# Optimization experiments

Hardware: AMD Instinct MI355X
Metric: run time of the kernel (lower is better)

The kernel has to match this reference:

```python
import jax, jax.numpy as jnp
import numpy as np

N_NODES = 100000
N_EDGES = 1600000
D = 128
N_LAYERS = 3
N_GRAPHS = 64
BN_EPS = 1e-5


def setup_inputs() -> dict:
    key = jax.random.key(0)
    ks = jax.random.split(key, 8)
    x = jax.random.normal(ks[0], (N_NODES, D), dtype=jnp.float32)
    edge_index = jax.random.randint(ks[1], (2, N_EDGES), 0, N_NODES, dtype=jnp.int64)
    batch = jnp.sort(jax.random.randint(ks[2], (N_NODES,), 0, N_GRAPHS, dtype=jnp.int64))
    scale = 1.0 / np.sqrt(D)
    W1 = jax.random.normal(ks[3], (N_LAYERS, D, D), dtype=jnp.float32) * scale
    W2 = jax.random.normal(ks[4], (N_LAYERS, D, D), dtype=jnp.float32) * scale
    g1 = jnp.ones((N_LAYERS, D), dtype=jnp.float32)
    b1 = jnp.zeros((N_LAYERS, D), dtype=jnp.float32)
    g2 = jnp.ones((N_LAYERS, D), dtype=jnp.float32)
    b2 = jnp.zeros((N_LAYERS, D), dtype=jnp.float32)
    eps = jnp.zeros((N_LAYERS,), dtype=jnp.float32)
    return {"x": x, "edge_index": edge_index, "batch": batch,
            "W1": W1, "g1": g1, "b1": b1, "W2": W2, "g2": g2, "b2": b2, "eps": eps}


def _batchnorm(z, gamma, beta):
    # BatchNorm1d in training mode: biased variance over the node dimension.
    mu = jnp.mean(z, axis=0, keepdims=True)
    var = jnp.mean(jnp.square(z - mu), axis=0, keepdims=True)
    return (z - mu) * jax.lax.rsqrt(var + BN_EPS) * gamma + beta


def reference(x, edge_index, batch, W1, g1, b1, W2, g2, b2, eps):
    src, dst = edge_index[0], edge_index[1]
    h = x
    for l in range(N_LAYERS):
        # GIN aggregation: sum of neighbor features via edge-index scatter-add
        agg = jax.ops.segment_sum(h[src], dst, num_segments=N_NODES)
        z = (1.0 + eps[l]) * h + agg
        # MLP: Linear(no bias) -> BN -> ReLU -> Linear(no bias) -> BN
        z = _batchnorm(z @ W1[l], g1[l], b1[l])
        z = jax.nn.relu(z)
        z = _batchnorm(z @ W2[l], g2[l], b2[l])
        h = jax.nn.relu(z)  # gnn_non_linear
    node_emb = h
    # mean readout per graph
    counts = jax.ops.segment_sum(jnp.ones((N_NODES,), dtype=h.dtype), batch, num_segments=N_GRAPHS)
    graph_sum = jax.ops.segment_sum(h, batch, num_segments=N_GRAPHS)
    graph_emb = graph_sum / jnp.maximum(counts, 1.0)[:, None]
    # emb_normalize -> F.normalize(p=2, dim=-1)
    graph_emb = graph_emb / jnp.maximum(jnp.linalg.norm(graph_emb, axis=-1, keepdims=True), 1e-12)
    return node_emb, graph_emb
```

## Files before the change

### kernel.cpp

```cpp
#include <hip/hip_runtime.h>

#define N_NODES 100000
#define N_EDGES 1600000
#define D 128
#define N_GRAPHS 64
#define BN_EPS 1e-5f
#define NSLICE 16

#define BNODES 256
#define NBUCK ((N_NODES + BNODES - 1) / BNODES)
#define EPB 8192
#define NABLK ((N_EDGES + EPB - 1) / EPB)

typedef short short8 __attribute__((ext_vector_type(8)));
typedef float f32x4 __attribute__((ext_vector_type(4)));

__device__ inline unsigned short f2bf(float f) {
  unsigned int u = __float_as_uint(f);
  u += 0x7fffu + ((u >> 16) & 1);
  return (unsigned short)(u >> 16);
}
__device__ inline float bf2f(unsigned short h) {
  return __uint_as_float(((unsigned int)h) << 16);
}
__device__ inline void unpack8(uint4 u, float* f) {
  f[0] = __uint_as_float(u.x << 16); f[1] = __uint_as_float(u.x & 0xffff0000u);
  f[2] = __uint_as_float(u.y << 16); f[3] = __uint_as_float(u.y & 0xffff0000u);
  f[4] = __uint_as_float(u.z << 16); f[5] = __uint_as_float(u.z & 0xffff0000u);
  f[6] = __uint_as_float(u.w << 16); f[7] = __uint_as_float(u.w & 0xffff0000u);
}
__device__ inline uint4 pack8(const float* f) {
  uint4 u;
  u.x = f2bf(f[0]) | ((unsigned)f2bf(f[1]) << 16);
  u.y = f2bf(f[2]) | ((unsigned)f2bf(f[3]) << 16);
  u.z = f2bf(f[4]) | ((unsigned)f2bf(f[5]) << 16);
  u.w = f2bf(f[6]) | ((unsigned)f2bf(f[7]) << 16);
  return u;
}

__global__ __launch_bounds__(256) void k_cast(const float* __restrict__ in,
                                              unsigned short* __restrict__ o) {
  long i = ((long)blockIdx.x * blockDim.x + threadIdx.x) * 8;
  if (i >= (long)N_NODES * D) return;
  float4 a = *(const float4*)(in + i);
  float4 b = *(const float4*)(in + i + 4);
  float f[8] = {a.x, a.y, a.z, a.w, b.x, b.y, b.z, b.w};
  *(uint4*)(o + i) = pack8(f);
}

__global__ __launch_bounds__(128) void k_wprep(const float* __restrict__ W1,
                                               const float* __restrict__ W2,
                                               unsigned short* __restrict__ Wt) {
  int m = blockIdx.x;
  int n = blockIdx.y;
  int k = threadIdx.x;
  int l = m >> 1, s = m & 1;
  const float* W = (s == 0 ? W1 : W2) + (size_t)l * D * D;
  Wt[((size_t)m * D + n) * D + k] = f2bf(W[(size_t)k * D + n]);
}

__global__ __launch_bounds__(256) void k_histb(const int* __restrict__ dst,
                                               int* __restrict__ ecount) {
  __shared__ int lh[NBUCK];
  const int t = threadIdx.x;
  const int e0 = blockIdx.x * EPB;
  const int e1 = min(e0 + EPB, N_EDGES);
  for (int i = t; i < NBUCK; i += 256) lh[i] = 0;
  __syncthreads();
  for (int e = e0 + t; e < e1; e += 256) atomicAdd(&lh[dst[e] >> 8], 1);
  __syncthreads();
  for (int i = t; i < NBUCK; i += 256)
    if (lh[i]) atomicAdd(&ecount[i], lh[i]);
}

__global__ __launch_bounds__(512) void k_scanb(const int* __restrict__ ecount,
                                               int* __restrict__ ebase,
                                               int* __restrict__ gcur) {
  __shared__ int ls[512];
  int t = threadIdx.x;
  int v = (t < NBUCK) ? ecount[t] : 0;
  ls[t] = v;
  __syncthreads();
  for (int o = 1; o < 512; o <<= 1) {
    int u = (t >= o) ? ls[t - o] : 0;
    __syncthreads();
    ls[t] += u;
    __syncthreads();
  }
  int ex = ls[t] - v;
  if (t < NBUCK) { ebase[t] = ex; gcur[t] = ex; }
  if (t == 0) ebase[NBUCK] = N_EDGES;
}

__global__ __launch_bounds__(256) void k_scatA(const int* __restrict__ ei,
                                               int* __restrict__ gcur,
                                               int2* __restrict__ pairs) {
  __shared__ int lh[NBUCK];
  __shared__ int lbase[NBUCK];
  const int t = threadIdx.x;
  const int e0 = blockIdx.x * EPB;
  const int e1 = min(e0 + EPB, N_EDGES);
  for (int i = t; i < NBUCK; i += 256) lh[i] = 0;
  __syncthreads();
  for (int e = e0 + t; e < e1; e += 256) atomicAdd(&lh[ei[N_EDGES + e] >> 8], 1);
  __syncthreads();
  for (int i = t; i < NBUCK; i += 256)
    lbase[i] = (lh[i] > 0) ? atomicAdd(&gcur[i], lh[i]) : 0;
  __syncthreads();
  for (int e = e0 + t; e < e1; e += 256) {
    int s = ei[e];
    int d = ei[N_EDGES + e];
    int p = atomicAdd(&lbase[d >> 8], 1);
    pairs[p] = make_int2(s, d);
  }
}

__global__ __launch_bounds__(256) void k_scatB(const int2* __restrict__ pairs,
                                               const int* __restrict__ ebase,
                                               int* __restrict__ off,
                                               int* __restrict__ esrc) {
  __shared__ int lcnt[BNODES];
  __shared__ int ls[256];
  const int t = threadIdx.x;
  const int b = blockIdx.x;
  const int nb0 = b * BNODES;
  const int nn = min(BNODES, N_NODES - nb0);
  const int s0 = ebase[b], s1 = ebase[b + 1];
  if (t < nn) lcnt[t] = 0;
  __syncthreads();
  for (int e = s0 + t; e < s1; e += 256) atomicAdd(&lcnt[pairs[e].y - nb0], 1);
  __syncthreads();
  int c0 = (t < nn) ? lcnt[t] : 0;
  ls[t] = c0;
  __syncthreads();
  for (int o = 1; o < 256; o <<= 1) {
    int u = (t >= o) ? ls[t - o] : 0;
    __syncthreads();
    ls[t] += u;
    __syncthreads();
  }
  int pre = ls[t] - c0;
  if (t < nn) {
    off[nb0 + t] = s0 + pre;
    lcnt[t] = s0 + pre;
  }
  __syncthreads();
  for (int e = s0 + t; e < s1; e += 256) {
    int2 p = pairs[e];
    int pos = atomicAdd(&lcnt[p.y - nb0], 1);
    esrc[pos] = p.x;
  }
  if (b == 0 && t == 0) off[N_NODES] = N_EDGES;
}

__global__ __launch_bounds__(256) void k_aggz(const unsigned short* __restrict__ h,
                                              const int* __restrict__ off,
                                              const int* __restrict__ esrc,
                                              const float* __restrict__ epsp,
                                              unsigned short* __restrict__ z) {
  const int lane = threadIdx.x & 63;
  const int n = blockIdx.x * 4 + (threadIdx.x >> 6);
  const int es = lane >> 4;
  const int fl = lane & 15;
  const int c = fl << 3;
  const float e = 1.0f + epsp[0];
  const int o0 = off[n], o1 = off[n + 1];

  float acc[8];
#pragma unroll
  for (int q = 0; q < 8; q++) acc[q] = 0.f;

  int j = o0;
  for (; j + 4 <= o1; j += 4) {
    int s = esrc[j + es];
    uint4 u = *(const uint4*)(h + (size_t)s * D + c);
    float f[8];
    unpack8(u, f);
#pragma unroll
    for (int q = 0; q < 8; q++) acc[q] += f[q];
  }
  if (es < o1 - j) {
    int s = esrc[j + es];
    uint4 u = *(const uint4*)(h + (size_t)s * D + c);
    float f[8];
    unpack8(u, f);
#pragma unroll
    for (int q = 0; q < 8; q++) acc[q] += f[q];
  }
#pragma unroll
  for (int q = 0; q < 8; q++) {
    acc[q] += __shfl_xor(acc[q], 16, 64);
    acc[q] += __shfl_xor(acc[q], 32, 64);
  }
  {
    uint4 u = *(const uint4*)(h + (size_t)n * D + c);
    float f[8];
    unpack8(u, f);
#pragma unroll
    for (int q = 0; q < 8; q++) acc[q] = fmaf(e, f[q], acc[q]);
  }
  if (es == 0) *(uint4*)(z + (size_t)n * D + c) = pack8(acc);
}

__global__ __launch_bounds__(256) void k_ew(const unsigned short* __restrict__ y,
                                            const float* __restrict__ sc,
                                            const float* __restrict__ tb,
                                            unsigned short* __restrict__ o) {
  long i = ((long)blockIdx.x * 256 + threadIdx.x) * 8;
  if (i >= (long)N_NODES * D) return;
  int cb = (int)(i & 127);
  uint4 u = *(const uint4*)(y + i);
  float f[8];
  unpack8(u, f);
#pragma unroll
  for (int q = 0; q < 8; q++) f[q] = fmaxf(fmaf(f[q], sc[cb + q], tb[cb + q]), 0.f);
  *(uint4*)(o + i) = pack8(f);
}

template <int MODE>
__global__ __launch_bounds__(256) void k_gemm(const unsigned short* __restrict__ A,
                                              const unsigned short* __restrict__ Wt,
                                              unsigned short* __restrict__ out,
                                              const float* __restrict__ sc,
                                              const float* __restrict__ tb,
                                              float* __restrict__ ssum,
                                              float* __restrict__ ssq) {
  __shared__ unsigned short Zs[64 * 136];
  __shared__ float psum[16 * 128];
  __shared__ float psq[16 * 128];
  const int t = threadIdx.x;
  const int row0 = blockIdx.x * 64;

#pragma unroll
  for (int i = 0; i < 4; i++) {
    int q = t + i * 256;
    int r = q >> 4, cb = (q & 15) << 3;
    int grow = row0 + r;
    uint4 u = make_uint4(0u, 0u, 0u, 0u);
    if (grow < N_NODES) {
      u = *(const uint4*)(A + (size_t)grow * D + cb);
      if (MODE == 1) {
        float f[8];
        unpack8(u, f);
#pragma unroll
        for (int jj = 0; jj < 8; jj++)
          f[jj] = fmaxf(fmaf(f[jj], sc[cb + jj], tb[cb + jj]), 0.f);
        u = pack8(f);
      }
    }
    *(uint4*)&Zs[r * 136 + cb] = u;
  }
  __syncthreads();

  const int lane = t & 63;
  const int wave = t >> 6;
  const int quad = lane >> 4;
  const int lr = lane & 15;
  const int m0 = wave * 16;

  f32x4 acc[8];
#pragma unroll
  for (int i = 0; i < 8; i++) acc[i] = (f32x4){0.f, 0.f, 0.f, 0.f};

#pragma unroll
  for (int kc = 0; kc < 128; kc += 32) {
    short8 af = *(const short8*)&Zs[(m0 + lr) * 136 + kc + quad * 8];
#pragma unroll
    for (int nt = 0; nt < 8; nt++) {
      short8 bf = *(const short8*)(Wt + (size_t)(nt * 16 + lr) * D + kc + quad * 8);
      acc[nt] = __builtin_amdgcn_mfma_f32_16x16x32_bf16(af, bf, acc[nt], 0, 0, 0);
    }
  }

#pragma unroll
  for (int nt = 0; nt < 8; nt++) {
    int col = nt * 16 + lr;
    float s = acc[nt][0] + acc[nt][1] + acc[nt][2] + acc[nt][3];
    float qq = acc[nt][0] * acc[nt][0] + acc[nt][1] * acc[nt][1] +
               acc[nt][2] * acc[nt][2] + acc[nt][3] * acc[nt][3];
    int gi = (wave * 4 + quad) * 128 + col;
    psum[gi] = s;
    psq[gi] = qq;
  }

#pragma unroll
  for (int rr = 0; rr < 4; rr++) {
    int grow = row0 + m0 + quad * 4 + rr;
    if (grow < N_NODES) {
#pragma unroll
      for (int nt = 0; nt < 8; nt++)
        out[(size_t)grow * D + nt * 16 + lr] = f2bf(acc[nt][rr]);
    }
  }

  __syncthreads();
  if (t < 128) {
    float S = 0.f, Q = 0.f;
#pragma unroll
    for (int i = 0; i < 16; i++) {
      S += psum[i * 128 + t];
      Q += psq[i * 128 + t];
    }
    int slice = blockIdx.x & (NSLICE - 1);
    atomicAdd(&ssum[slice * 128 + t], S);
    atomicAdd(&ssq[slice * 128 + t], Q);
  }
}

__global__ void k_bnfin(const float* __restrict__ ssum, const float* __restrict__ ssq,
                        const float* __restrict__ gamma, const float* __restrict__ beta,
                        float* __restrict__ sc, float* __restrict__ tb) {
  int f = threadIdx.x;
  float S = 0.f, Q = 0.f;
  for (int i = 0; i < NSLICE; i++) { S += ssum[i * 128 + f]; Q += ssq[i * 128 + f]; }
  float m = S * (1.0f / (float)N_NODES);
  float v = Q * (1.0f / (float)N_NODES) - m * m;
  float r = rsqrtf(v + BN_EPS);
  float s = r * gamma[f];
  sc[f] = s;
  tb[f] = beta[f] - m * s;
}

#define RCH 64
__global__ __launch_bounds__(128) void k_readout(const unsigned short* __restrict__ y,
                                                 const int* __restrict__ batch,
                                                 const float* __restrict__ sc,
                                                 const float* __restrict__ tb,
                                                 float* __restrict__ node_out,
                                                 float* __restrict__ gsum,
                                                 int* __restrict__ gcnt) {
  int start = blockIdx.x * RCH;
  int end = min(start + RCH, N_NODES);
  if (start >= end) return;
  int f = threadIdx.x;
  float s = sc[f], tt = tb[f];
  float acc = 0.f;
  int cnt = 0;
  int curg = batch[start];
  for (int n = start; n < end; n++) {
    int gg = batch[n];
    float v = fmaxf(fmaf(bf2f(y[(size_t)n * D + f]), s, tt), 0.f);
    node_out[(size_t)n * D + f] = v;
    if (gg != curg) {
      atomicAdd(&gsum[curg * D + f], acc);
      if (f == 0) atomicAdd(&gcnt[curg], cnt);
      acc = 0.f; cnt = 0; curg = gg;
    }
    acc += v;
    cnt++;
  }
  atomicAdd(&gsum[curg * D + f], acc);
  if (f == 0) atomicAdd(&gcnt[curg], cnt);
}

__global__ __launch_bounds__(128) void k_gnorm(const float* __restrict__ gsum,
                                               const int* __restrict__ gcnt,
                                               float* __restrict__ out) {
  __shared__ float red[128];
  int g = blockIdx.x, f = threadIdx.x;
  float c = (float)gcnt[g];
  float v = gsum[g * D + f] / fmaxf(c, 1.0f);
  red[f] = v * v;
  __syncthreads();
  for (int o = 64; o > 0; o >>= 1) {
    if (f < o) red[f] += red[f + o];
    __syncthreads();
  }
  float nrm = sqrtf(red[0]);
  out[(size_t)g * D + f] = v / fmaxf(nrm, 1e-12f);
}

extern "C" void kernel_launch(void* const* d_in, const int* in_sizes, int n_in,
                              void* d_out, int out_size, void* d_ws, size_t ws_size,
                              hipStream_t stream) {
  const float* x   = (const float*)d_in[0];
  const int*   ei  = (const int*)d_in[1];
  const int*   bat = (const int*)d_in[2];
  const float* W1  = (const float*)d_in[3];
  const float* g1  = (const float*)d_in[4];
  const float* b1  = (const float*)d_in[5];
  const float* W2  = (const float*)d_in[6];
  const float* g2  = (const float*)d_in[7];
  const float* b2  = (const float*)d_in[8];
  const float* eps = (const float*)d_in[9];
  float* out = (float*)d_out;

  char* w = (char*)d_ws;
  const size_t FEAT_B = (size_t)N_NODES * D * 2;
  unsigned short* xb   = (unsigned short*)w; w += FEAT_B;
  unsigned short* bufA = (unsigned short*)w; w += FEAT_B;
  unsigned short* bufB = (unsigned short*)w; w += FEAT_B;
  unsigned short* bufC = (unsigned short*)w; w += FEAT_B;
  unsigned short* WtB  = (unsigned short*)w; w += (size_t)6 * D * D * 2;
  int* off   = (int*)w; w += 400016;
  int* ebase = (int*)w; w += 2048;
  int* gcur  = (int*)w; w += 2048;
  int* esrc  = (int*)w; w += (size_t)N_EDGES * 4;
  float* sc1 = (float*)w; w += 512;
  float* tb1 = (float*)w; w += 512;
  float* sc2 = (float*)w; w += 512;
  float* tb2 = (float*)w; w += 512;
  char* zreg = w;
  int* ecount  = (int*)w; w += 2048;
  float* stats = (float*)w; w += (size_t)6 * 2 * NSLICE * 128 * 4;
  float* gsum  = (float*)w; w += (size_t)N_GRAPHS * D * 4;
  int* gcnt    = (int*)w; w += 256;
  size_t zbytes = (size_t)((char*)w - zreg);
  int2* pairs = (int2*)bufB;

  hipMemsetAsync(zreg, 0, zbytes, stream);

  k_cast<<<(N_NODES * D / 8 + 255) / 256, 256, 0, stream>>>(x, xb);
  k_wprep<<<dim3(6, 128), 128, 0, stream>>>(W1, W2, WtB);

  k_histb<<<NABLK, 256, 0, stream>>>(ei + N_EDGES, ecount);
  k_scanb<<<1, 512, 0, stream>>>(ecount, ebase, gcur);
  k_scatA<<<NABLK, 256, 0, stream>>>(ei, gcur, pairs);
  k_scatB<<<NBUCK, 256, 0, stream>>>(pairs, ebase, off, esrc);

  const int gemm_grid = (N_NODES + 63) / 64;
  const int aggz_grid = N_NODES / 4;
  const int ew_grid = (N_NODES * D / 8 + 255) / 256;

  for (int l = 0; l < 3; l++) {
    float* s1 = stats + (size_t)(l * 2 + 0) * 2 * NSLICE * 128;
    float* q1 = s1 + NSLICE * 128;
    float* s2 = stats + (size_t)(l * 2 + 1) * 2 * NSLICE * 128;
    float* q2 = s2 + NSLICE * 128;
    if (l > 0) {
      k_ew<<<ew_grid, 256, 0, stream>>>(bufC, sc2, tb2, xb);
    }
    k_aggz<<<aggz_grid, 256, 0, stream>>>(xb, off, esrc, eps + l, bufA);
    k_gemm<0><<<gemm_grid, 256, 0, stream>>>(bufA, WtB + (size_t)(l * 2 + 0) * D * D, bufB,
                                             nullptr, nullptr, s1, q1);
    k_bnfin<<<1, 128, 0, stream>>>(s1, q1, g1 + (size_t)l * D, b1 + (size_t)l * D, sc1, tb1);
    k_gemm<1><<<gemm_grid, 256, 0, stream>>>(bufB, WtB + (size_t)(l * 2 + 1) * D * D, bufC,
                                             sc1, tb1, s2, q2);
    k_bnfin<<<1, 128, 0, stream>>>(s2, q2, g2 + (size_t)l * D, b2 + (size_t)l * D, sc2, tb2);
  }

  k_readout<<<(N_NODES + RCH - 1) / RCH, 128, 0, stream>>>(bufC, bat, sc2, tb2,
                                                           out, gsum, gcnt);
  k_gnorm<<<N_GRAPHS, 128, 0, stream>>>(gsum, gcnt, out + (size_t)N_NODES * D);
}
```

Before: 661.8 us.

## Fuse BN+ReLU into aggregation gather and drop LDS staging in GEMM

Removes the separate elementwise BN2+ReLU pass between layers by applying the scale/shift/ReLU to each gathered neighbor row inside the aggregation kernel. The GEMM now has each wave own an independent 16-row tile, loading its A fragments straight from global memory without LDS or block barriers, and reducing column statistics with wave shuffles before the atomics. The cost is recomputing BN+ReLU once per edge instead of once per node, plus more atomics per block. The GEMM also drops its row bounds check, which relies on N_NODES being a multiple of 16.

```diff
diff --git a/kernel.cpp b/kernel.cpp
--- a/kernel.cpp
+++ b/kernel.cpp
@@ -153,10 +153,13 @@
   if (b == 0 && t == 0) off[N_NODES] = N_EDGES;
 }
 
+template <int MODE>
 __global__ __launch_bounds__(256) void k_aggz(const unsigned short* __restrict__ h,
                                               const int* __restrict__ off,
                                               const int* __restrict__ esrc,
                                               const float* __restrict__ epsp,
+                                              const float* __restrict__ sc,
+                                              const float* __restrict__ tb,
                                               unsigned short* __restrict__ z) {
   const int lane = threadIdx.x & 63;
   const int n = blockIdx.x * 4 + (threadIdx.x >> 6);
@@ -166,6 +169,12 @@
   const float e = 1.0f + epsp[0];
   const int o0 = off[n], o1 = off[n + 1];
 
+  float S[8], T[8];
+  if (MODE == 1) {
+#pragma unroll
+    for (int q = 0; q < 8; q++) { S[q] = sc[c + q]; T[q] = tb[c + q]; }
+  }
+
   float acc[8];
 #pragma unroll
   for (int q = 0; q < 8; q++) acc[q] = 0.f;
@@ -177,7 +186,10 @@
     float f[8];
     unpack8(u, f);
 #pragma unroll
-    for (int q = 0; q < 8; q++) acc[q] += f[q];
+    for (int q = 0; q < 8; q++) {
+      if (MODE == 1) f[q] = fmaxf(fmaf(f[q], S[q], T[q]), 0.f);
+      acc[q] += f[q];
+    }
   }
   if (es < o1 - j) {
     int s = esrc[j + es];
@@ -185,7 +197,10 @@
     float f[8];
     unpack8(u, f);
 #pragma unroll
-    for (int q = 0; q < 8; q++) acc[q] += f[q];
+    for (int q = 0; q < 8; q++) {
+      if (MODE == 1) f[q] = fmaxf(fmaf(f[q], S[q], T[q]), 0.f);
+      acc[q] += f[q];
+    }
   }
 #pragma unroll
   for (int q = 0; q < 8; q++) {
@@ -197,24 +212,12 @@
     float f[8];
     unpack8(u, f);
 #pragma unroll
-    for (int q = 0; q < 8; q++) acc[q] = fmaf(e, f[q], acc[q]);
+    for (int q = 0; q < 8; q++) {
+      if (MODE == 1) f[q] = fmaxf(fmaf(f[q], S[q], T[q]), 0.f);
+      acc[q] = fmaf(e, f[q], acc[q]);
+    }
   }
   if (es == 0) *(uint4*)(z + (size_t)n * D + c) = pack8(acc);
-}
-
-__global__ __launch_bounds__(256) void k_ew(const unsigned short* __restrict__ y,
-                                            const float* __restrict__ sc,
-                                            const float* __restrict__ tb,
-                                            unsigned short* __restrict__ o) {
-  long i = ((long)blockIdx.x * 256 + threadIdx.x) * 8;
-  if (i >= (long)N_NODES * D) return;
-  int cb = (int)(i & 127);
-  uint4 u = *(const uint4*)(y + i);
-  float f[8];
-  unpack8(u, f);
-#pragma unroll
-  for (int q = 0; q < 8; q++) f[q] = fmaxf(fmaf(f[q], sc[cb + q], tb[cb + q]), 0.f);
-  *(uint4*)(o + i) = pack8(f);
 }
 
 template <int MODE>
@@ -225,38 +228,13 @@
                                               const float* __restrict__ tb,
                                               float* __restrict__ ssum,
                                               float* __restrict__ ssq) {
-  __shared__ unsigned short Zs[64 * 136];
-  __shared__ float psum[16 * 128];
-  __shared__ float psq[16 * 128];
   const int t = threadIdx.x;
-  const int row0 = blockIdx.x * 64;
-
-#pragma unroll
-  for (int i = 0; i < 4; i++) {
-    int q = t + i * 256;
-    int r = q >> 4, cb = (q & 15) << 3;
-    int grow = row0 + r;
-    uint4 u = make_uint4(0u, 0u, 0u, 0u);
-    if (grow < N_NODES) {
-      u = *(const uint4*)(A + (size_t)grow * D + cb);
-      if (MODE == 1) {
-        float f[8];
-        unpack8(u, f);
-#pragma unroll
-        for (int jj = 0; jj < 8; jj++)
-          f[jj] = fmaxf(fmaf(f[jj], sc[cb + jj], tb[cb + jj]), 0.f);
-        u = pack8(f);
-      }
-    }
-    *(uint4*)&Zs[r * 136 + cb] = u;
-  }
-  __syncthreads();
-
   const int lane = t & 63;
-  const int wave = t >> 6;
   const int quad = lane >> 4;
   const int lr = lane & 15;
-  const int m0 = wave * 16;
+  const int tile = blockIdx.x * 4 + (t >> 6);
+  if (tile >= N_NODES / 16) return;
+  const int row0 = tile * 16;
 
   f32x4 acc[8];
 #pragma unroll
@@ -264,46 +242,61 @@
 
 #pragma unroll
   for (int kc = 0; kc < 128; kc += 32) {
-    short8 af = *(const short8*)&Zs[(m0 + lr) * 136 + kc + quad * 8];
+    const int kb = kc + quad * 8;
+    uint4 ua = *(const uint4*)(A + (size_t)(row0 + lr) * D + kb);
+    if (MODE == 1) {
+      float f[8];
+      unpack8(ua, f);
+      float4 s0 = *(const float4*)(sc + kb);
+      float4 s1 = *(const float4*)(sc + kb + 4);
+      float4 t0 = *(const float4*)(tb + kb);
+      float4 t1 = *(const float4*)(tb + kb + 4);
+      f[0] = fmaxf(fmaf(f[0], s0.x, t0.x), 0.f);
+      f[1] = fmaxf(fmaf(f[1], s0.y, t0.y), 0.f);
+      f[2] = fmaxf(fmaf(f[2], s0.z, t0.z), 0.f);
+      f[3] = fmaxf(fmaf(f[3], s0.w, t0.w), 0.f);
+      f[4] = fmaxf(fmaf(f[4], s1.x, t1.x), 0.f);
+      f[5] = fmaxf(fmaf(f[5], s1.y, t1.y), 0.f);
+      f[6] = fmaxf(fmaf(f[6], s1.z, t1.z), 0.f);
+      f[7] = fmaxf(fmaf(f[7], s1.w, t1.w), 0.f);
+      ua = pack8(f);
+    }
+    short8 af = *(short8*)&ua;
 #pragma unroll
     for (int nt = 0; nt < 8; nt++) {
-      short8 bf = *(const short8*)(Wt + (size_t)(nt * 16 + lr) * D + kc + quad * 8);
+      uint4 ub = *(const uint4*)(Wt + (size_t)(nt * 16 + lr) * D + kb);
+      short8 bf = *(short8*)&ub;
       acc[nt] = __builtin_amdgcn_mfma_f32_16x16x32_bf16(af, bf, acc[nt], 0, 0, 0);
     }
   }
 
+  float S[8], Q[8];
 #pragma unroll
   for (int nt = 0; nt < 8; nt++) {
-    int col = nt * 16 + lr;
-    float s = acc[nt][0] + acc[nt][1] + acc[nt][2] + acc[nt][3];
-    float qq = acc[nt][0] * acc[nt][0] + acc[nt][1] * acc[nt][1] +
-               acc[nt][2] * acc[nt][2] + acc[nt][3] * acc[nt][3];
-    int gi = (wave * 4 + quad) * 128 + col;
-    psum[gi] = s;
-    psq[gi] = qq;
+    S[nt] = acc[nt][0] + acc[nt][1] + acc[nt][2] + acc[nt][3];
+    Q[nt] = acc[nt][0] * acc[nt][0] + acc[nt][1] * acc[nt][1] +
+            acc[nt][2] * acc[nt][2] + acc[nt][3] * acc[nt][3];
+    S[nt] += __shfl_xor(S[nt], 16, 64);
+    S[nt] += __shfl_xor(S[nt], 32, 64);
+    Q[nt] += __shfl_xor(Q[nt], 16, 64);
+    Q[nt] += __shfl_xor(Q[nt], 32, 64);
   }
 
 #pragma unroll
   for (int rr = 0; rr < 4; rr++) {
-    int grow = row0 + m0 + quad * 4 + rr;
-    if (grow < N_NODES) {
-#pragma unroll
-      for (int nt = 0; nt < 8; nt++)
-        out[(size_t)grow * D + nt * 16 + lr] = f2bf(acc[nt][rr]);
-    }
-  }
-
-  __syncthreads();
-  if (t < 128) {
-    float S = 0.f, Q = 0.f;
-#pragma unroll
-    for (int i = 0; i < 16; i++) {
-      S += psum[i * 128 + t];
-      Q += psq[i * 128 + t];
-    }
-    int slice = blockIdx.x & (NSLICE - 1);
-    atomicAdd(&ssum[slice * 128 + t], S);
-    atomicAdd(&ssq[slice * 128 + t], Q);
+    int grow = row0 + quad * 4 + rr;
+#pragma unroll
+    for (int nt = 0; nt < 8; nt++)
+      out[(size_t)grow * D + nt * 16 + lr] = f2bf(acc[nt][rr]);
+  }
+
+  if (quad == 0) {
+    int slice = tile & (NSLICE - 1);
+#pragma unroll
+    for (int nt = 0; nt < 8; nt++) {
+      atomicAdd(&ssum[slice * 128 + nt * 16 + lr], S[nt]);
+      atomicAdd(&ssq[slice * 128 + nt * 16 + lr], Q[nt]);
+    }
   }
 }
 
@@ -418,19 +411,21 @@
   k_scatA<<<NABLK, 256, 0, stream>>>(ei, gcur, pairs);
   k_scatB<<<NBUCK, 256, 0, stream>>>(pairs, ebase, off, esrc);
 
-  const int gemm_grid = (N_NODES + 63) / 64;
+  const int gemm_grid = (N_NODES / 16 + 3) / 4;
   const int aggz_grid = N_NODES / 4;
-  const int ew_grid = (N_NODES * D / 8 + 255) / 256;
 
   for (int l = 0; l < 3; l++) {
     float* s1 = stats + (size_t)(l * 2 + 0) * 2 * NSLICE * 128;
     float* q1 = s1 + NSLICE * 128;
     float* s2 = stats + (size_t)(l * 2 + 1) * 2 * NSLICE * 128;
     float* q2 = s2 + NSLICE * 128;
-    if (l > 0) {
-      k_ew<<<ew_grid, 256, 0, stream>>>(bufC, sc2, tb2, xb);
-    }
-    k_aggz<<<aggz_grid, 256, 0, stream>>>(xb, off, esrc, eps + l, bufA);
+    if (l == 0) {
+      k_aggz<0><<<aggz_grid, 256, 0, stream>>>(xb, off, esrc, eps + l,
+                                               nullptr, nullptr, bufA);
+    } else {
+      k_aggz<1><<<aggz_grid, 256, 0, stream>>>(bufC, off, esrc, eps + l,
+                                               sc2, tb2, bufA);
+    }
     k_gemm<0><<<gemm_grid, 256, 0, stream>>>(bufA, WtB + (size_t)(l * 2 + 0) * D * D, bufB,
                                              nullptr, nullptr, s1, q1);
     k_bnfin<<<1, 128, 0, stream>>>(s1, q1, g1 + (size_t)l * D, b1 + (size_t)l * D, sc1, tb1);
```

New measurement: 716.1 us. 8.2% more time.
